# Kernel tuning notes

Measured on AMD Instinct MI355X. Metric: run time of the kernel, lower is better.

Reference implementation:

```python
import jax, jax.numpy as jnp
import numpy as np

NUM_HEADS = 12
EPSILON = 1e-6
SCORE_SCALE = 1.0


def setup_inputs() -> dict:
    key = jax.random.key(0)
    ks = jax.random.split(key, 5)
    B, L, E = 2, 2048, 768
    x = jax.random.normal(ks[0], (B, L, E), dtype=jnp.float32)
    attention_mask = jnp.ones((B, L), dtype=jnp.int32)
    # linear params (lecun-ish scale)
    Wqkv = jax.random.normal(ks[1], (E, 3 * E), dtype=jnp.float32) / np.sqrt(E)
    bqkv = jnp.zeros((3 * E,), dtype=jnp.float32)
    Wout = jax.random.normal(ks[2], (E, E), dtype=jnp.float32) / np.sqrt(E)
    bout = jnp.zeros((E,), dtype=jnp.float32)
    return {"x": x, "attention_mask": attention_mask, "Wqkv": Wqkv,
            "bqkv": bqkv, "Wout": Wout, "bout": bout}


def reference(x, attention_mask, Wqkv, bqkv, Wout, bout):
    B, L, E = x.shape
    H = NUM_HEADS
    D = E // H
    qkv = x @ Wqkv + bqkv                      # [B,L,3E]
    q, k, v = jnp.split(qkv, 3, axis=-1)
    q = q.reshape(B, L, H, D).transpose(0, 2, 1, 3)  # [B,H,L,D]
    k = k.reshape(B, L, H, D).transpose(0, 2, 1, 3)
    v = v.reshape(B, L, H, D).transpose(0, 2, 1, 3)

    dot = jnp.einsum('bhid,bhjd->bhij', q, k)        # [B,H,L,L]
    q_sq = jnp.sum(q * q, axis=-1)[..., :, None]     # [B,H,L,1]
    k_sq = jnp.sum(k * k, axis=-1)[..., None, :]     # [B,H,1,L]
    scores = (dot * dot) / (q_sq + k_sq - 2.0 * dot + EPSILON)
    scores = scores * SCORE_SCALE

    pad = attention_mask[:, None, None, :]           # [B,1,1,L]
    scores = jnp.where(pad == 1, scores, jnp.finfo(scores.dtype).min)

    attn = jax.nn.softmax(scores, axis=-1)
    out = jnp.einsum('bhij,bhjd->bhid', attn, v)     # [B,H,L,D]
    out = out.transpose(0, 2, 1, 3).reshape(B, L, E)
    return out @ Wout + bout
```

## Files before the change

### kernel.cpp

```cpp
#include <hip/hip_runtime.h>
#include <hip/hip_bf16.h>
#include <cstdint>
#include <cstddef>


typedef __bf16 bf16_t;
typedef __bf16 bf16x8 __attribute__((ext_vector_type(8)));
typedef __bf16 bf16x4 __attribute__((ext_vector_type(4)));
typedef float floatx4 __attribute__((ext_vector_type(4)));

#define DEVI static __device__ __forceinline__

#define Bc 2
#define Lc 2048
#define Ec 768
#define Hc 12
#define Dc 64
#define N3c 2304
#define Mc 4096
#define ROWSc (Bc * Hc * Lc)

DEVI void glds16(const bf16_t* g, bf16_t* l) {
  __builtin_amdgcn_global_load_lds(
      (const __attribute__((address_space(1))) void*)g,
      (__attribute__((address_space(3))) void*)l, 16, 0, 0);
}


__global__ __launch_bounds__(256) void k_cvt(const float* __restrict__ in,
                                             bf16_t* __restrict__ out, int n) {
  int i = (blockIdx.x * 256 + threadIdx.x) * 4;
  if (i >= n) return;
  float4 v = *(const float4*)(in + i);
  bf16x4 o;
  o[0] = (bf16_t)v.x; o[1] = (bf16_t)v.y; o[2] = (bf16_t)v.z; o[3] = (bf16_t)v.w;
  *(bf16x4*)(out + i) = o;
}

__global__ __launch_bounds__(256) void k_tc(const float* __restrict__ in,
                                            bf16_t* __restrict__ out, int R, int C) {
  __shared__ float tile[32][33];
  int c0 = blockIdx.x * 32, r0 = blockIdx.y * 32;
  int tx = threadIdx.x, ty = threadIdx.y;
  #pragma unroll
  for (int i = 0; i < 32; i += 8)
    tile[ty + i][tx] = in[(size_t)(r0 + ty + i) * C + c0 + tx];
  __syncthreads();
  #pragma unroll
  for (int i = 0; i < 32; i += 8)
    out[(size_t)(c0 + ty + i) * R + r0 + tx] = (bf16_t)tile[tx][ty + i];
}


DEVI void gemm_core(const bf16_t* __restrict__ A, const bf16_t* __restrict__ Bt,
                    bf16_t* lA, bf16_t* lB, int m0, int n0, floatx4 (&acc)[4][4]) {
  const int tid = threadIdx.x, wave = tid >> 6, lane = tid & 63;
  const int wm = (wave >> 1) * 64, wn = (wave & 1) * 64;
  const int lrow = lane >> 2, lseg = lane & 3;
  const int quad = lane >> 4, r16 = lane & 15;
  for (int kk = 0; kk < 768; kk += 32) {
    glds16(A  + (size_t)(m0 + wave * 32      + lrow) * 768 + kk + lseg * 8, lA + (wave * 32) * 32);
    glds16(A  + (size_t)(m0 + wave * 32 + 16 + lrow) * 768 + kk + lseg * 8, lA + (wave * 32 + 16) * 32);
    glds16(Bt + (size_t)(n0 + wave * 32      + lrow) * 768 + kk + lseg * 8, lB + (wave * 32) * 32);
    glds16(Bt + (size_t)(n0 + wave * 32 + 16 + lrow) * 768 + kk + lseg * 8, lB + (wave * 32 + 16) * 32);
    __syncthreads();
    bf16x8 af[4], bv[4];
    #pragma unroll
    for (int mi = 0; mi < 4; mi++)
      af[mi] = *(const bf16x8*)(lA + (wm + mi * 16 + r16) * 32 + quad * 8);
    #pragma unroll
    for (int ni = 0; ni < 4; ni++)
      bv[ni] = *(const bf16x8*)(lB + (wn + ni * 16 + r16) * 32 + quad * 8);
    #pragma unroll
    for (int mi = 0; mi < 4; mi++)
      #pragma unroll
      for (int ni = 0; ni < 4; ni++)
        acc[mi][ni] = __builtin_amdgcn_mfma_f32_16x16x32_bf16(af[mi], bv[ni], acc[mi][ni], 0, 0, 0);
    __syncthreads();
  }
}

__global__ __launch_bounds__(256) void k_gemm_qkv(
    const bf16_t* __restrict__ A, const bf16_t* __restrict__ Bt,
    const float* __restrict__ bias,
    bf16_t* __restrict__ Qo, bf16_t* __restrict__ Ko, bf16_t* __restrict__ Vo) {
  __shared__ bf16_t lA[128 * 32];
  __shared__ bf16_t lB[128 * 32];
  const int m0 = blockIdx.y * 128, n0 = blockIdx.x * 128;
  const int tid = threadIdx.x, wave = tid >> 6, lane = tid & 63;
  const int wm = (wave >> 1) * 64, wn = (wave & 1) * 64;
  const int quad = lane >> 4, r16 = lane & 15;
  floatx4 acc[4][4] = {};
  gemm_core(A, Bt, lA, lB, m0, n0, acc);

  const int sec = n0 / 768;
  bf16_t* dst = (sec == 0) ? Qo : ((sec == 1) ? Ko : Vo);
  #pragma unroll
  for (int ni = 0; ni < 4; ni++) {
    const int n = n0 + wn + ni * 16 + r16;
    const int nn = n - sec * 768;
    const int h = nn >> 6, d = nn & 63;
    const float bvs = bias[n];
    #pragma unroll
    for (int mi = 0; mi < 4; mi++) {
      #pragma unroll
      for (int reg = 0; reg < 4; reg++) {
        const int m = m0 + wm + mi * 16 + quad * 4 + reg;
        const int b = m >> 11, l = m & 2047;
        const float v = acc[mi][ni][reg] + bvs;
        dst[(((size_t)(b * Hc + h)) * Lc + l) * Dc + d] = (bf16_t)v;
      }
    }
  }
}

__global__ __launch_bounds__(256) void k_gemm_out(
    const bf16_t* __restrict__ A, const bf16_t* __restrict__ Bt,
    const float* __restrict__ bias, float* __restrict__ out) {
  __shared__ bf16_t lA[128 * 32];
  __shared__ bf16_t lB[128 * 32];
  const int m0 = blockIdx.y * 128, n0 = blockIdx.x * 128;
  const int tid = threadIdx.x, wave = tid >> 6, lane = tid & 63;
  const int wm = (wave >> 1) * 64, wn = (wave & 1) * 64;
  const int quad = lane >> 4, r16 = lane & 15;
  floatx4 acc[4][4] = {};
  gemm_core(A, Bt, lA, lB, m0, n0, acc);
  #pragma unroll
  for (int ni = 0; ni < 4; ni++) {
    const int n = n0 + wn + ni * 16 + r16;
    const float bvs = bias[n];
    #pragma unroll
    for (int mi = 0; mi < 4; mi++) {
      #pragma unroll
      for (int reg = 0; reg < 4; reg++) {
        const int m = m0 + wm + mi * 16 + quad * 4 + reg;
        out[(size_t)m * Ec + n] = acc[mi][ni][reg] + bvs;
      }
    }
  }
}

__global__ __launch_bounds__(256) void k_sq(const bf16_t* __restrict__ Q,
                                            const bf16_t* __restrict__ K,
                                            float* __restrict__ qsq, float* __restrict__ ksq) {
  const int row = blockIdx.x * 256 + threadIdx.x;
  const bf16x8* q = (const bf16x8*)(Q + (size_t)row * 64);
  const bf16x8* k = (const bf16x8*)(K + (size_t)row * 64);
  float sq = 0.f, sk = 0.f;
  #pragma unroll
  for (int c = 0; c < 8; c++) {
    bf16x8 vq = q[c], vk = k[c];
    #pragma unroll
    for (int j = 0; j < 8; j++) {
      float a = (float)vq[j]; sq += a * a;
      float b = (float)vk[j]; sk += b * b;
    }
  }
  qsq[row] = sq;
  ksq[row] = sk + 1e-6f;
}

__global__ __launch_bounds__(256) void k_vt(const bf16_t* __restrict__ V,
                                            bf16_t* __restrict__ VT) {
  __shared__ bf16_t t[64][72];
  const int gid = blockIdx.x;
  const int bh = gid >> 5, j0 = (gid & 31) * 64;
  const int tid = threadIdx.x;
  const bf16_t* Vh = V + ((size_t)bh * Lc) * Dc;
  bf16_t* VTh = VT + ((size_t)bh * Dc) * Lc;
  #pragma unroll
  for (int it = 0; it < 2; ++it) {
    int c = tid + it * 256;
    int j = c >> 3, seg = c & 7;
    *(bf16x8*)&t[j][seg * 8] = *(const bf16x8*)(Vh + (size_t)(j0 + j) * 64 + seg * 8);
  }
  __syncthreads();
  #pragma unroll
  for (int it = 0; it < 2; ++it) {
    int c = tid + it * 256;
    int d = c >> 3, jseg = c & 7;
    bf16x8 o;
    #pragma unroll
    for (int u = 0; u < 8; u++) o[u] = t[jseg * 8 + u][d];
    *(bf16x8*)(VTh + (size_t)d * Lc + j0 + jseg * 8) = o;
  }
}

__global__ __launch_bounds__(256) void k_attn(
    const bf16_t* __restrict__ Q, const bf16_t* __restrict__ K,
    const bf16_t* __restrict__ VT, const float* __restrict__ qsq,
    const float* __restrict__ ksq, const int* __restrict__ mask,
    float* __restrict__ Op, float* __restrict__ Mp, float* __restrict__ Lp,
    int nS) {
  __shared__ bf16_t lK[2][4096];
  __shared__ bf16_t lV[2][4096];
  __shared__ bf16_t lP[4][16 * 72];
  const int gid = blockIdx.x;
  const int s = blockIdx.y;
  const int bh = gid >> 5, qt = gid & 31;
  const int b = bh / Hc;
  const int tid = threadIdx.x, wave = tid >> 6, lane = tid & 63;
  const int quad = lane >> 4, r16 = lane & 15;
  const int q0 = qt * 64 + wave * 16;
  const bf16_t* Qh = Q + ((size_t)bh * Lc) * Dc;
  const bf16_t* Kh = K + ((size_t)bh * Lc) * Dc;
  const bf16_t* VTh = VT + ((size_t)bh * Dc) * Lc;
  const float* qsqh = qsq + bh * Lc;
  const float* ksqh = ksq + bh * Lc;
  const int* maskb = mask + b * Lc;
  bf16_t* myP = &lP[wave][0];

  const int kt_lo = (32 * s) / nS * 64;
  const int kt_hi = (32 * (s + 1)) / nS * 64;
  const int nt = (kt_hi - kt_lo) >> 6;

  const int p0 = wave * 64 + lane;
  const int srow = p0 >> 3;
  const int sj = (p0 & 7) ^ (srow & 7);
  const bf16_t* kg0 = Kh + (size_t)(kt_lo + srow) * 64 + sj * 8;
  const bf16_t* kg1 = kg0 + 32 * 64;
  const bf16_t* vg0 = VTh + (size_t)srow * Lc + kt_lo + sj * 8;
  const bf16_t* vg1 = vg0 + 32 * Lc;
  const int ld0 = wave * 64 * 8, ld1 = (256 + wave * 64) * 8;

  const int sl0 = ((quad ^ (r16 & 7)) * 8);
  const int sl1 = sl0 ^ 32;

  bf16x8 qf0 = *(const bf16x8*)(Qh + (size_t)(q0 + r16) * 64 + quad * 8);
  bf16x8 qf1 = *(const bf16x8*)(Qh + (size_t)(q0 + r16) * 64 + 32 + quad * 8);
  const float qs = qsqh[q0 + r16];
  float mi = -1e30f, li = 0.f;
  floatx4 of[4] = {};

  glds16(kg0, &lK[0][ld0]);
  glds16(kg1, &lK[0][ld1]);
  glds16(vg0, &lV[0][ld0]);
  glds16(vg1, &lV[0][ld1]);
  kg0 += 4096; kg1 += 4096; vg0 += 64; vg1 += 64;
  __syncthreads();

  for (int t = 0; t < nt; t++) {
    const int cur = t & 1;
    if (t + 1 < nt) {
      const int nxt = cur ^ 1;
      glds16(kg0, &lK[nxt][ld0]);
      glds16(kg1, &lK[nxt][ld1]);
      glds16(vg0, &lV[nxt][ld0]);
      glds16(vg1, &lV[nxt][ld1]);
      kg0 += 4096; kg1 += 4096; vg0 += 64; vg1 += 64;
    }
    const int kt = kt_lo + t * 64;
    float4 ks4[4];
    int4 mk4[4];
    #pragma unroll
    for (int c = 0; c < 4; c++) {
      ks4[c] = *(const float4*)(ksqh + kt + c * 16 + quad * 4);
      mk4[c] = *(const int4*)(maskb + kt + c * 16 + quad * 4);
    }
    floatx4 dot[4];
    #pragma unroll
    for (int c = 0; c < 4; c++) {
      const int rbase = (c * 16 + r16) * 64;
      bf16x8 kf0 = *(const bf16x8*)(&lK[cur][rbase + sl0]);
      bf16x8 kf1 = *(const bf16x8*)(&lK[cur][rbase + sl1]);
      floatx4 a = {};
      a = __builtin_amdgcn_mfma_f32_16x16x32_bf16(kf0, qf0, a, 0, 0, 0);
      a = __builtin_amdgcn_mfma_f32_16x16x32_bf16(kf1, qf1, a, 0, 0, 0);
      dot[c] = a;
    }
    float sv[4][4];
    float rmax = -1e30f;
    #pragma unroll
    for (int c = 0; c < 4; c++) {
      #pragma unroll
      for (int reg = 0; reg < 4; reg++) {
        const float dd = dot[c][reg];
        const float kss = ((const float*)&ks4[c])[reg];
        const int mk = ((const int*)&mk4[c])[reg];
        const float den = qs + kss - 2.f * dd;
        float sc = dd * dd * __builtin_amdgcn_rcpf(den);
        sc = (mk == 1) ? sc : -1e30f;
        sv[c][reg] = sc;
        rmax = fmaxf(rmax, sc);
      }
    }
    rmax = fmaxf(rmax, __shfl_xor(rmax, 16));
    rmax = fmaxf(rmax, __shfl_xor(rmax, 32));
    const float mnew = fmaxf(mi, rmax);
    const float alpha = __expf(mi - mnew);
    float psum = 0.f;
    #pragma unroll
    for (int c = 0; c < 4; c++) {
      bf16x4 pk;
      #pragma unroll
      for (int reg = 0; reg < 4; reg++) {
        const float p = __expf(sv[c][reg] - mnew);
        psum += p;
        pk[reg] = (bf16_t)p;
      }
      *(bf16x4*)(myP + r16 * 72 + c * 16 + quad * 4) = pk;
    }
    psum += __shfl_xor(psum, 16);
    psum += __shfl_xor(psum, 32);
    li = li * alpha + psum;
    mi = mnew;
    #pragma unroll
    for (int t4 = 0; t4 < 4; t4++) {
      #pragma unroll
      for (int reg = 0; reg < 4; reg++) of[t4][reg] *= alpha;
    }
    bf16x8 pf0 = *(const bf16x8*)(myP + r16 * 72 + quad * 8);
    bf16x8 pf1 = *(const bf16x8*)(myP + r16 * 72 + 32 + quad * 8);
    #pragma unroll
    for (int t4 = 0; t4 < 4; t4++) {
      const int rbase = (t4 * 16 + r16) * 64;
      bf16x8 vf0 = *(const bf16x8*)(&lV[cur][rbase + sl0]);
      bf16x8 vf1 = *(const bf16x8*)(&lV[cur][rbase + sl1]);
      of[t4] = __builtin_amdgcn_mfma_f32_16x16x32_bf16(vf0, pf0, of[t4], 0, 0, 0);
      of[t4] = __builtin_amdgcn_mfma_f32_16x16x32_bf16(vf1, pf1, of[t4], 0, 0, 0);
    }
    __syncthreads();
  }
  const size_t idx = (size_t)s * ROWSc + (size_t)bh * Lc + q0 + r16;
  #pragma unroll
  for (int t4 = 0; t4 < 4; t4++)
    *(float4*)(Op + idx * 64 + t4 * 16 + quad * 4) =
        make_float4(of[t4][0], of[t4][1], of[t4][2], of[t4][3]);
  if (lane < 16) { Mp[idx] = mi; Lp[idx] = li; }
}

__global__ __launch_bounds__(256) void k_merge(
    const float* __restrict__ Op, const float* __restrict__ Mp,
    const float* __restrict__ Lp, bf16_t* __restrict__ AO, int nS) {
  const int t = blockIdx.x * 256 + threadIdx.x;
  const int row = t >> 4, dc = (t & 15) * 4;
  float mmax = -1e30f;
  for (int s = 0; s < nS; s++) mmax = fmaxf(mmax, Mp[(size_t)s * ROWSc + row]);
  float L = 0.f;
  float o0 = 0.f, o1 = 0.f, o2 = 0.f, o3 = 0.f;
  for (int s = 0; s < nS; s++) {
    const size_t idx = (size_t)s * ROWSc + row;
    const float w = __expf(Mp[idx] - mmax);
    L += w * Lp[idx];
    const float4 v = *(const float4*)(Op + idx * 64 + dc);
    o0 += w * v.x; o1 += w * v.y; o2 += w * v.z; o3 += w * v.w;
  }
  const float inv = (L > 0.f) ? __builtin_amdgcn_rcpf(L) : 0.f;
  const int bh = row >> 11, l = row & 2047;
  const int b = bh / Hc, h = bh - b * Hc;
  bf16x4 o;
  o[0] = (bf16_t)(o0 * inv); o[1] = (bf16_t)(o1 * inv);
  o[2] = (bf16_t)(o2 * inv); o[3] = (bf16_t)(o3 * inv);
  *(bf16x4*)(AO + ((size_t)(b * Lc + l)) * Ec + h * 64 + dc) = o;
}


extern "C" void kernel_launch(void* const* d_in, const int* in_sizes, int n_in,
                              void* d_out, int out_size, void* d_ws, size_t ws_size,
                              hipStream_t stream) {
  const float* x    = (const float*)d_in[0];
  const int*   mask = (const int*)d_in[1];
  const float* Wqkv = (const float*)d_in[2];
  const float* bqkv = (const float*)d_in[3];
  const float* Wout = (const float*)d_in[4];
  const float* bout = (const float*)d_in[5];
  float* out = (float*)d_out;

  auto al = [](size_t x) { return (x + 255) & ~(size_t)255; };
  char* ws = (char*)d_ws;
  size_t off = 0;
  auto carve = [&](size_t bytes) -> char* {
    char* p = ws + off;
    off += al(bytes);
    return p;
  };
  bf16_t* WoT = (bf16_t*)carve((size_t)Ec * Ec * 2);
  bf16_t* Qb  = (bf16_t*)carve((size_t)ROWSc * Dc * 2);
  bf16_t* Kb  = (bf16_t*)carve((size_t)ROWSc * Dc * 2);
  bf16_t* VTb = (bf16_t*)carve((size_t)ROWSc * Dc * 2);
  bf16_t* AOb = (bf16_t*)carve((size_t)Mc * Ec * 2);
  float*  qsq = (float*)carve((size_t)ROWSc * 4);
  float*  ksq = (float*)carve((size_t)ROWSc * 4);
  const size_t uni = off;
  bf16_t* xb  = (bf16_t*)(ws + uni);
  bf16_t* WqT = (bf16_t*)(ws + uni + al((size_t)Mc * Ec * 2));
  bf16_t* Vb  = (bf16_t*)(ws + uni + al((size_t)Mc * Ec * 2) + al((size_t)N3c * Ec * 2));
  const size_t ph1 = al((size_t)Mc * Ec * 2) + al((size_t)N3c * Ec * 2) + al((size_t)ROWSc * Dc * 2);
  auto ph2 = [&](int S) {
    return al((size_t)S * ROWSc * Dc * 4) + 2 * al((size_t)S * ROWSc * 4);
  };
  int S = 1;
  {
    size_t need = uni + (ph1 > ph2(2) ? ph1 : ph2(2));
    if (need <= ws_size) S = 2;
  }
  float* Op = (float*)(ws + uni);
  float* Mp = (float*)(ws + uni + al((size_t)S * ROWSc * Dc * 4));
  float* Lp = (float*)(ws + uni + al((size_t)S * ROWSc * Dc * 4) + al((size_t)S * ROWSc * 4));
  (void)in_sizes; (void)n_in; (void)out_size;

  k_cvt<<<(Mc * Ec / 4 + 255) / 256, 256, 0, stream>>>(x, xb, Mc * Ec);
  k_tc<<<dim3(N3c / 32, Ec / 32), dim3(32, 8), 0, stream>>>(Wqkv, WqT, Ec, N3c);
  k_tc<<<dim3(Ec / 32, Ec / 32), dim3(32, 8), 0, stream>>>(Wout, WoT, Ec, Ec);
  k_gemm_qkv<<<dim3(N3c / 128, Mc / 128), 256, 0, stream>>>(xb, WqT, bqkv, Qb, Kb, Vb);
  k_sq<<<ROWSc / 256, 256, 0, stream>>>(Qb, Kb, qsq, ksq);
  k_vt<<<ROWSc / 64, 256, 0, stream>>>(Vb, VTb);
  k_attn<<<dim3(ROWSc / 64, S), 256, 0, stream>>>(Qb, Kb, VTb, qsq, ksq, mask, Op, Mp, Lp, S);
  k_merge<<<ROWSc * 16 / 256, 256, 0, stream>>>(Op, Mp, Lp, AOb, S);
  k_gemm_out<<<dim3(Ec / 128, Mc / 128), 256, 0, stream>>>(AOb, WoT, bout, out);
}
```

Before: 219.3 us.

## Fuse V transpose, mask, and split-K merge into neighbouring kernels

The QKV GEMM epilogue now writes V directly in transposed layout with 4-wide stores, removing the separate transpose kernel. The padding mask is folded into the k-squared array as a negative sentinel, so the attention kernel no longer loads the mask per tile. Attention drops the two-way key split and the merge kernel, normalising and writing bf16 output directly. This removes the partial-output round trip and two launches, but halves the grid of the attention kernel, which can cost occupancy and load balance.

```diff
diff --git a/kernel.cpp b/kernel.cpp
--- a/kernel.cpp
+++ b/kernel.cpp
@@ -83,7 +83,7 @@
 __global__ __launch_bounds__(256) void k_gemm_qkv(
     const bf16_t* __restrict__ A, const bf16_t* __restrict__ Bt,
     const float* __restrict__ bias,
-    bf16_t* __restrict__ Qo, bf16_t* __restrict__ Ko, bf16_t* __restrict__ Vo) {
+    bf16_t* __restrict__ Qo, bf16_t* __restrict__ Ko, bf16_t* __restrict__ VTo) {
   __shared__ bf16_t lA[128 * 32];
   __shared__ bf16_t lB[128 * 32];
   const int m0 = blockIdx.y * 128, n0 = blockIdx.x * 128;
@@ -94,21 +94,40 @@
   gemm_core(A, Bt, lA, lB, m0, n0, acc);
 
   const int sec = n0 / 768;
-  bf16_t* dst = (sec == 0) ? Qo : ((sec == 1) ? Ko : Vo);
-  #pragma unroll
-  for (int ni = 0; ni < 4; ni++) {
-    const int n = n0 + wn + ni * 16 + r16;
-    const int nn = n - sec * 768;
-    const int h = nn >> 6, d = nn & 63;
-    const float bvs = bias[n];
-    #pragma unroll
-    for (int mi = 0; mi < 4; mi++) {
-      #pragma unroll
-      for (int reg = 0; reg < 4; reg++) {
-        const int m = m0 + wm + mi * 16 + quad * 4 + reg;
+  if (sec == 2) {
+    #pragma unroll
+    for (int ni = 0; ni < 4; ni++) {
+      const int n = n0 + wn + ni * 16 + r16;
+      const int nn = n - 1536;
+      const int h = nn >> 6, d = nn & 63;
+      const float bvs = bias[n];
+      #pragma unroll
+      for (int mi = 0; mi < 4; mi++) {
+        const int m = m0 + wm + mi * 16 + quad * 4;
         const int b = m >> 11, l = m & 2047;
-        const float v = acc[mi][ni][reg] + bvs;
-        dst[(((size_t)(b * Hc + h)) * Lc + l) * Dc + d] = (bf16_t)v;
+        bf16x4 o;
+        #pragma unroll
+        for (int reg = 0; reg < 4; reg++) o[reg] = (bf16_t)(acc[mi][ni][reg] + bvs);
+        *(bf16x4*)(VTo + ((size_t)(b * Hc + h) * Dc + d) * Lc + l) = o;
+      }
+    }
+  } else {
+    bf16_t* dst = (sec == 0) ? Qo : Ko;
+    #pragma unroll
+    for (int ni = 0; ni < 4; ni++) {
+      const int n = n0 + wn + ni * 16 + r16;
+      const int nn = n - sec * 768;
+      const int h = nn >> 6, d = nn & 63;
+      const float bvs = bias[n];
+      #pragma unroll
+      for (int mi = 0; mi < 4; mi++) {
+        #pragma unroll
+        for (int reg = 0; reg < 4; reg++) {
+          const int m = m0 + wm + mi * 16 + quad * 4 + reg;
+          const int b = m >> 11, l = m & 2047;
+          const float v = acc[mi][ni][reg] + bvs;
+          dst[(((size_t)(b * Hc + h)) * Lc + l) * Dc + d] = (bf16_t)v;
+        }
       }
     }
   }
@@ -142,6 +161,7 @@
 
 __global__ __launch_bounds__(256) void k_sq(const bf16_t* __restrict__ Q,
                                             const bf16_t* __restrict__ K,
+                                            const int* __restrict__ mask,
                                             float* __restrict__ qsq, float* __restrict__ ksq) {
   const int row = blockIdx.x * 256 + threadIdx.x;
   const bf16x8* q = (const bf16x8*)(Q + (size_t)row * 64);
@@ -156,49 +176,23 @@
       float b = (float)vk[j]; sk += b * b;
     }
   }
+  const int bh = row >> 11, l = row & 2047;
+  const int b = bh / Hc;
+  const int mk = mask[b * Lc + l];
   qsq[row] = sq;
-  ksq[row] = sk + 1e-6f;
-}
-
-__global__ __launch_bounds__(256) void k_vt(const bf16_t* __restrict__ V,
-                                            bf16_t* __restrict__ VT) {
-  __shared__ bf16_t t[64][72];
-  const int gid = blockIdx.x;
-  const int bh = gid >> 5, j0 = (gid & 31) * 64;
-  const int tid = threadIdx.x;
-  const bf16_t* Vh = V + ((size_t)bh * Lc) * Dc;
-  bf16_t* VTh = VT + ((size_t)bh * Dc) * Lc;
-  #pragma unroll
-  for (int it = 0; it < 2; ++it) {
-    int c = tid + it * 256;
-    int j = c >> 3, seg = c & 7;
-    *(bf16x8*)&t[j][seg * 8] = *(const bf16x8*)(Vh + (size_t)(j0 + j) * 64 + seg * 8);
-  }
-  __syncthreads();
-  #pragma unroll
-  for (int it = 0; it < 2; ++it) {
-    int c = tid + it * 256;
-    int d = c >> 3, jseg = c & 7;
-    bf16x8 o;
-    #pragma unroll
-    for (int u = 0; u < 8; u++) o[u] = t[jseg * 8 + u][d];
-    *(bf16x8*)(VTh + (size_t)d * Lc + j0 + jseg * 8) = o;
-  }
+  ksq[row] = (mk == 1) ? (sk + 1e-6f) : -1e30f;
 }
 
 __global__ __launch_bounds__(256) void k_attn(
     const bf16_t* __restrict__ Q, const bf16_t* __restrict__ K,
     const bf16_t* __restrict__ VT, const float* __restrict__ qsq,
-    const float* __restrict__ ksq, const int* __restrict__ mask,
-    float* __restrict__ Op, float* __restrict__ Mp, float* __restrict__ Lp,
-    int nS) {
+    const float* __restrict__ ksq, bf16_t* __restrict__ AO) {
   __shared__ bf16_t lK[2][4096];
   __shared__ bf16_t lV[2][4096];
   __shared__ bf16_t lP[4][16 * 72];
   const int gid = blockIdx.x;
-  const int s = blockIdx.y;
   const int bh = gid >> 5, qt = gid & 31;
-  const int b = bh / Hc;
+  const int b = bh / Hc, h = bh - b * Hc;
   const int tid = threadIdx.x, wave = tid >> 6, lane = tid & 63;
   const int quad = lane >> 4, r16 = lane & 15;
   const int q0 = qt * 64 + wave * 16;
@@ -207,19 +201,14 @@
   const bf16_t* VTh = VT + ((size_t)bh * Dc) * Lc;
   const float* qsqh = qsq + bh * Lc;
   const float* ksqh = ksq + bh * Lc;
-  const int* maskb = mask + b * Lc;
   bf16_t* myP = &lP[wave][0];
-
-  const int kt_lo = (32 * s) / nS * 64;
-  const int kt_hi = (32 * (s + 1)) / nS * 64;
-  const int nt = (kt_hi - kt_lo) >> 6;
 
   const int p0 = wave * 64 + lane;
   const int srow = p0 >> 3;
   const int sj = (p0 & 7) ^ (srow & 7);
-  const bf16_t* kg0 = Kh + (size_t)(kt_lo + srow) * 64 + sj * 8;
+  const bf16_t* kg0 = Kh + (size_t)srow * 64 + sj * 8;
   const bf16_t* kg1 = kg0 + 32 * 64;
-  const bf16_t* vg0 = VTh + (size_t)srow * Lc + kt_lo + sj * 8;
+  const bf16_t* vg0 = VTh + (size_t)srow * Lc + sj * 8;
   const bf16_t* vg1 = vg0 + 32 * Lc;
   const int ld0 = wave * 64 * 8, ld1 = (256 + wave * 64) * 8;
 
@@ -239,6 +228,7 @@
   kg0 += 4096; kg1 += 4096; vg0 += 64; vg1 += 64;
   __syncthreads();
 
+  const int nt = Lc / 64;
   for (int t = 0; t < nt; t++) {
     const int cur = t & 1;
     if (t + 1 < nt) {
@@ -249,14 +239,11 @@
       glds16(vg1, &lV[nxt][ld1]);
       kg0 += 4096; kg1 += 4096; vg0 += 64; vg1 += 64;
     }
-    const int kt = kt_lo + t * 64;
+    const int kt = t * 64;
     float4 ks4[4];
-    int4 mk4[4];
-    #pragma unroll
-    for (int c = 0; c < 4; c++) {
+    #pragma unroll
+    for (int c = 0; c < 4; c++)
       ks4[c] = *(const float4*)(ksqh + kt + c * 16 + quad * 4);
-      mk4[c] = *(const int4*)(maskb + kt + c * 16 + quad * 4);
-    }
     floatx4 dot[4];
     #pragma unroll
     for (int c = 0; c < 4; c++) {
@@ -276,10 +263,9 @@
       for (int reg = 0; reg < 4; reg++) {
         const float dd = dot[c][reg];
         const float kss = ((const float*)&ks4[c])[reg];
-        const int mk = ((const int*)&mk4[c])[reg];
         const float den = qs + kss - 2.f * dd;
         float sc = dd * dd * __builtin_amdgcn_rcpf(den);
-        sc = (mk == 1) ? sc : -1e30f;
+        sc = (kss < 0.f) ? -1e30f : sc;
         sv[c][reg] = sc;
         rmax = fmaxf(rmax, sc);
       }
@@ -321,37 +307,16 @@
     }
     __syncthreads();
   }
-  const size_t idx = (size_t)s * ROWSc + (size_t)bh * Lc + q0 + r16;
-  #pragma unroll
-  for (int t4 = 0; t4 < 4; t4++)
-    *(float4*)(Op + idx * 64 + t4 * 16 + quad * 4) =
-        make_float4(of[t4][0], of[t4][1], of[t4][2], of[t4][3]);
-  if (lane < 16) { Mp[idx] = mi; Lp[idx] = li; }
-}
-
-__global__ __launch_bounds__(256) void k_merge(
-    const float* __restrict__ Op, const float* __restrict__ Mp,
-    const float* __restrict__ Lp, bf16_t* __restrict__ AO, int nS) {
-  const int t = blockIdx.x * 256 + threadIdx.x;
-  const int row = t >> 4, dc = (t & 15) * 4;
-  float mmax = -1e30f;
-  for (int s = 0; s < nS; s++) mmax = fmaxf(mmax, Mp[(size_t)s * ROWSc + row]);
-  float L = 0.f;
-  float o0 = 0.f, o1 = 0.f, o2 = 0.f, o3 = 0.f;
-  for (int s = 0; s < nS; s++) {
-    const size_t idx = (size_t)s * ROWSc + row;
-    const float w = __expf(Mp[idx] - mmax);
-    L += w * Lp[idx];
-    const float4 v = *(const float4*)(Op + idx * 64 + dc);
-    o0 += w * v.x; o1 += w * v.y; o2 += w * v.z; o3 += w * v.w;
-  }
-  const float inv = (L > 0.f) ? __builtin_amdgcn_rcpf(L) : 0.f;
-  const int bh = row >> 11, l = row & 2047;
-  const int b = bh / Hc, h = bh - b * Hc;
-  bf16x4 o;
-  o[0] = (bf16_t)(o0 * inv); o[1] = (bf16_t)(o1 * inv);
-  o[2] = (bf16_t)(o2 * inv); o[3] = (bf16_t)(o3 * inv);
-  *(bf16x4*)(AO + ((size_t)(b * Lc + l)) * Ec + h * 64 + dc) = o;
+  const float inv = (li > 0.f) ? __builtin_amdgcn_rcpf(li) : 0.f;
+  const int l = q0 + r16;
+  bf16_t* aor = AO + ((size_t)(b * Lc + l)) * Ec + h * 64;
+  #pragma unroll
+  for (int t4 = 0; t4 < 4; t4++) {
+    bf16x4 o;
+    #pragma unroll
+    for (int reg = 0; reg < 4; reg++) o[reg] = (bf16_t)(of[t4][reg] * inv);
+    *(bf16x4*)(aor + t4 * 16 + quad * 4) = o;
+  }
 }
 
 
@@ -366,7 +331,7 @@
   const float* bout = (const float*)d_in[5];
   float* out = (float*)d_out;
 
-  auto al = [](size_t x) { return (x + 255) & ~(size_t)255; };
+  auto al = [](size_t v) { return (v + 255) & ~(size_t)255; };
   char* ws = (char*)d_ws;
   size_t off = 0;
   auto carve = [&](size_t bytes) -> char* {
@@ -381,31 +346,15 @@
   bf16_t* AOb = (bf16_t*)carve((size_t)Mc * Ec * 2);
   float*  qsq = (float*)carve((size_t)ROWSc * 4);
   float*  ksq = (float*)carve((size_t)ROWSc * 4);
-  const size_t uni = off;
-  bf16_t* xb  = (bf16_t*)(ws + uni);
-  bf16_t* WqT = (bf16_t*)(ws + uni + al((size_t)Mc * Ec * 2));
-  bf16_t* Vb  = (bf16_t*)(ws + uni + al((size_t)Mc * Ec * 2) + al((size_t)N3c * Ec * 2));
-  const size_t ph1 = al((size_t)Mc * Ec * 2) + al((size_t)N3c * Ec * 2) + al((size_t)ROWSc * Dc * 2);
-  auto ph2 = [&](int S) {
-    return al((size_t)S * ROWSc * Dc * 4) + 2 * al((size_t)S * ROWSc * 4);
-  };
-  int S = 1;
-  {
-    size_t need = uni + (ph1 > ph2(2) ? ph1 : ph2(2));
-    if (need <= ws_size) S = 2;
-  }
-  float* Op = (float*)(ws + uni);
-  float* Mp = (float*)(ws + uni + al((size_t)S * ROWSc * Dc * 4));
-  float* Lp = (float*)(ws + uni + al((size_t)S * ROWSc * Dc * 4) + al((size_t)S * ROWSc * 4));
-  (void)in_sizes; (void)n_in; (void)out_size;
+  bf16_t* xb  = (bf16_t*)carve((size_t)Mc * Ec * 2);
+  bf16_t* WqT = (bf16_t*)carve((size_t)N3c * Ec * 2);
+  (void)in_sizes; (void)n_in; (void)out_size; (void)ws_size;
 
   k_cvt<<<(Mc * Ec / 4 + 255) / 256, 256, 0, stream>>>(x, xb, Mc * Ec);
   k_tc<<<dim3(N3c / 32, Ec / 32), dim3(32, 8), 0, stream>>>(Wqkv, WqT, Ec, N3c);
   k_tc<<<dim3(Ec / 32, Ec / 32), dim3(32, 8), 0, stream>>>(Wout, WoT, Ec, Ec);
-  k_gemm_qkv<<<dim3(N3c / 128, Mc / 128), 256, 0, stream>>>(xb, WqT, bqkv, Qb, Kb, Vb);
-  k_sq<<<ROWSc / 256, 256, 0, stream>>>(Qb, Kb, qsq, ksq);
-  k_vt<<<ROWSc / 64, 256, 0, stream>>>(Vb, VTb);
-  k_attn<<<dim3(ROWSc / 64, S), 256, 0, stream>>>(Qb, Kb, VTb, qsq, ksq, mask, Op, Mp, Lp, S);
-  k_merge<<<ROWSc * 16 / 256, 256, 0, stream>>>(Op, Mp, Lp, AOb, S);
+  k_gemm_qkv<<<dim3(N3c / 128, Mc / 128), 256, 0, stream>>>(xb, WqT, bqkv, Qb, Kb, VTb);
+  k_sq<<<ROWSc / 256, 256, 0, stream>>>(Qb, Kb, mask, qsq, ksq);
+  k_attn<<<ROWSc / 64, 256, 0, stream>>>(Qb, Kb, VTb, qsq, ksq, AOb);
   k_gemm_out<<<dim3(Ec / 128, Mc / 128), 256, 0, stream>>>(AOb, WoT, bout, out);
 }
```

Result: slower. 253.4 us (+15.5%).

## Write V transposed from QKV GEMM epilogue and fold mask into ksq

Applied to the files above, without the earlier changes.

The QKV GEMM epilogue now writes the V section directly in transposed [B,H,D,L] layout with 4-wide bf16 stores, which removes the separate k_vt transpose kernel and its V round-trip through memory. The padding mask is folded into the ksq buffer as a negative sentinel in k_sq, so the attention kernel no longer loads the mask per key tile. The cost is that the Q/K epilogue keeps its scattered scalar stores, and the sentinel check assumes ksq is never otherwise negative.

```diff
diff --git a/kernel.cpp b/kernel.cpp
--- a/kernel.cpp
+++ b/kernel.cpp
@@ -83,7 +83,7 @@
 __global__ __launch_bounds__(256) void k_gemm_qkv(
     const bf16_t* __restrict__ A, const bf16_t* __restrict__ Bt,
     const float* __restrict__ bias,
-    bf16_t* __restrict__ Qo, bf16_t* __restrict__ Ko, bf16_t* __restrict__ Vo) {
+    bf16_t* __restrict__ Qo, bf16_t* __restrict__ Ko, bf16_t* __restrict__ VTo) {
   __shared__ bf16_t lA[128 * 32];
   __shared__ bf16_t lB[128 * 32];
   const int m0 = blockIdx.y * 128, n0 = blockIdx.x * 128;
@@ -94,21 +94,40 @@
   gemm_core(A, Bt, lA, lB, m0, n0, acc);
 
   const int sec = n0 / 768;
-  bf16_t* dst = (sec == 0) ? Qo : ((sec == 1) ? Ko : Vo);
-  #pragma unroll
-  for (int ni = 0; ni < 4; ni++) {
-    const int n = n0 + wn + ni * 16 + r16;
-    const int nn = n - sec * 768;
-    const int h = nn >> 6, d = nn & 63;
-    const float bvs = bias[n];
-    #pragma unroll
-    for (int mi = 0; mi < 4; mi++) {
-      #pragma unroll
-      for (int reg = 0; reg < 4; reg++) {
-        const int m = m0 + wm + mi * 16 + quad * 4 + reg;
+  if (sec == 2) {
+    #pragma unroll
+    for (int ni = 0; ni < 4; ni++) {
+      const int n = n0 + wn + ni * 16 + r16;
+      const int nn = n - 1536;
+      const int h = nn >> 6, d = nn & 63;
+      const float bvs = bias[n];
+      #pragma unroll
+      for (int mi = 0; mi < 4; mi++) {
+        const int m = m0 + wm + mi * 16 + quad * 4;
         const int b = m >> 11, l = m & 2047;
-        const float v = acc[mi][ni][reg] + bvs;
-        dst[(((size_t)(b * Hc + h)) * Lc + l) * Dc + d] = (bf16_t)v;
+        bf16x4 o;
+        #pragma unroll
+        for (int reg = 0; reg < 4; reg++) o[reg] = (bf16_t)(acc[mi][ni][reg] + bvs);
+        *(bf16x4*)(VTo + ((size_t)(b * Hc + h) * Dc + d) * Lc + l) = o;
+      }
+    }
+  } else {
+    bf16_t* dst = (sec == 0) ? Qo : Ko;
+    #pragma unroll
+    for (int ni = 0; ni < 4; ni++) {
+      const int n = n0 + wn + ni * 16 + r16;
+      const int nn = n - sec * 768;
+      const int h = nn >> 6, d = nn & 63;
+      const float bvs = bias[n];
+      #pragma unroll
+      for (int mi = 0; mi < 4; mi++) {
+        #pragma unroll
+        for (int reg = 0; reg < 4; reg++) {
+          const int m = m0 + wm + mi * 16 + quad * 4 + reg;
+          const int b = m >> 11, l = m & 2047;
+          const float v = acc[mi][ni][reg] + bvs;
+          dst[(((size_t)(b * Hc + h)) * Lc + l) * Dc + d] = (bf16_t)v;
+        }
       }
     }
   }
@@ -142,6 +161,7 @@
 
 __global__ __launch_bounds__(256) void k_sq(const bf16_t* __restrict__ Q,
                                             const bf16_t* __restrict__ K,
+                                            const int* __restrict__ mask,
                                             float* __restrict__ qsq, float* __restrict__ ksq) {
   const int row = blockIdx.x * 256 + threadIdx.x;
   const bf16x8* q = (const bf16x8*)(Q + (size_t)row * 64);
@@ -156,40 +176,17 @@
       float b = (float)vk[j]; sk += b * b;
     }
   }
+  const int bh = row >> 11, l = row & 2047;
+  const int b = bh / Hc;
+  const int mk = mask[b * Lc + l];
   qsq[row] = sq;
-  ksq[row] = sk + 1e-6f;
-}
-
-__global__ __launch_bounds__(256) void k_vt(const bf16_t* __restrict__ V,
-                                            bf16_t* __restrict__ VT) {
-  __shared__ bf16_t t[64][72];
-  const int gid = blockIdx.x;
-  const int bh = gid >> 5, j0 = (gid & 31) * 64;
-  const int tid = threadIdx.x;
-  const bf16_t* Vh = V + ((size_t)bh * Lc) * Dc;
-  bf16_t* VTh = VT + ((size_t)bh * Dc) * Lc;
-  #pragma unroll
-  for (int it = 0; it < 2; ++it) {
-    int c = tid + it * 256;
-    int j = c >> 3, seg = c & 7;
-    *(bf16x8*)&t[j][seg * 8] = *(const bf16x8*)(Vh + (size_t)(j0 + j) * 64 + seg * 8);
-  }
-  __syncthreads();
-  #pragma unroll
-  for (int it = 0; it < 2; ++it) {
-    int c = tid + it * 256;
-    int d = c >> 3, jseg = c & 7;
-    bf16x8 o;
-    #pragma unroll
-    for (int u = 0; u < 8; u++) o[u] = t[jseg * 8 + u][d];
-    *(bf16x8*)(VTh + (size_t)d * Lc + j0 + jseg * 8) = o;
-  }
+  ksq[row] = (mk == 1) ? (sk + 1e-6f) : -1e30f;
 }
 
 __global__ __launch_bounds__(256) void k_attn(
     const bf16_t* __restrict__ Q, const bf16_t* __restrict__ K,
     const bf16_t* __restrict__ VT, const float* __restrict__ qsq,
-    const float* __restrict__ ksq, const int* __restrict__ mask,
+    const float* __restrict__ ksq,
     float* __restrict__ Op, float* __restrict__ Mp, float* __restrict__ Lp,
     int nS) {
   __shared__ bf16_t lK[2][4096];
@@ -198,7 +195,6 @@
   const int gid = blockIdx.x;
   const int s = blockIdx.y;
   const int bh = gid >> 5, qt = gid & 31;
-  const int b = bh / Hc;
   const int tid = threadIdx.x, wave = tid >> 6, lane = tid & 63;
   const int quad = lane >> 4, r16 = lane & 15;
   const int q0 = qt * 64 + wave * 16;
@@ -207,7 +203,6 @@
   const bf16_t* VTh = VT + ((size_t)bh * Dc) * Lc;
   const float* qsqh = qsq + bh * Lc;
   const float* ksqh = ksq + bh * Lc;
-  const int* maskb = mask + b * Lc;
   bf16_t* myP = &lP[wave][0];
 
   const int kt_lo = (32 * s) / nS * 64;
@@ -251,12 +246,9 @@
     }
     const int kt = kt_lo + t * 64;
     float4 ks4[4];
-    int4 mk4[4];
-    #pragma unroll
-    for (int c = 0; c < 4; c++) {
+    #pragma unroll
+    for (int c = 0; c < 4; c++)
       ks4[c] = *(const float4*)(ksqh + kt + c * 16 + quad * 4);
-      mk4[c] = *(const int4*)(maskb + kt + c * 16 + quad * 4);
-    }
     floatx4 dot[4];
     #pragma unroll
     for (int c = 0; c < 4; c++) {
@@ -276,10 +268,9 @@
       for (int reg = 0; reg < 4; reg++) {
         const float dd = dot[c][reg];
         const float kss = ((const float*)&ks4[c])[reg];
-        const int mk = ((const int*)&mk4[c])[reg];
         const float den = qs + kss - 2.f * dd;
         float sc = dd * dd * __builtin_amdgcn_rcpf(den);
-        sc = (mk == 1) ? sc : -1e30f;
+        sc = (kss < 0.f) ? -1e30f : sc;
         sv[c][reg] = sc;
         rmax = fmaxf(rmax, sc);
       }
@@ -366,7 +357,7 @@
   const float* bout = (const float*)d_in[5];
   float* out = (float*)d_out;
 
-  auto al = [](size_t x) { return (x + 255) & ~(size_t)255; };
+  auto al = [](size_t v) { return (v + 255) & ~(size_t)255; };
   char* ws = (char*)d_ws;
   size_t off = 0;
   auto carve = [&](size_t bytes) -> char* {
@@ -384,8 +375,7 @@
   const size_t uni = off;
   bf16_t* xb  = (bf16_t*)(ws + uni);
   bf16_t* WqT = (bf16_t*)(ws + uni + al((size_t)Mc * Ec * 2));
-  bf16_t* Vb  = (bf16_t*)(ws + uni + al((size_t)Mc * Ec * 2) + al((size_t)N3c * Ec * 2));
-  const size_t ph1 = al((size_t)Mc * Ec * 2) + al((size_t)N3c * Ec * 2) + al((size_t)ROWSc * Dc * 2);
+  const size_t ph1 = al((size_t)Mc * Ec * 2) + al((size_t)N3c * Ec * 2);
   auto ph2 = [&](int S) {
     return al((size_t)S * ROWSc * Dc * 4) + 2 * al((size_t)S * ROWSc * 4);
   };
@@ -402,10 +392,9 @@
   k_cvt<<<(Mc * Ec / 4 + 255) / 256, 256, 0, stream>>>(x, xb, Mc * Ec);
   k_tc<<<dim3(N3c / 32, Ec / 32), dim3(32, 8), 0, stream>>>(Wqkv, WqT, Ec, N3c);
   k_tc<<<dim3(Ec / 32, Ec / 32), dim3(32, 8), 0, stream>>>(Wout, WoT, Ec, Ec);
-  k_gemm_qkv<<<dim3(N3c / 128, Mc / 128), 256, 0, stream>>>(xb, WqT, bqkv, Qb, Kb, Vb);
-  k_sq<<<ROWSc / 256, 256, 0, stream>>>(Qb, Kb, qsq, ksq);
-  k_vt<<<ROWSc / 64, 256, 0, stream>>>(Vb, VTb);
-  k_attn<<<dim3(ROWSc / 64, S), 256, 0, stream>>>(Qb, Kb, VTb, qsq, ksq, mask, Op, Mp, Lp, S);
+  k_gemm_qkv<<<dim3(N3c / 128, Mc / 128), 256, 0, stream>>>(xb, WqT, bqkv, Qb, Kb, VTb);
+  k_sq<<<ROWSc / 256, 256, 0, stream>>>(Qb, Kb, mask, qsq, ksq);
+  k_attn<<<dim3(ROWSc / 64, S), 256, 0, stream>>>(Qb, Kb, VTb, qsq, ksq, Op, Mp, Lp, S);
   k_merge<<<ROWSc * 16 / 256, 256, 0, stream>>>(Op, Mp, Lp, AOb, S);
   k_gemm_out<<<dim3(Ec / 128, Mc / 128), 256, 0, stream>>>(AOb, WoT, bout, out);
 }
```

Result: slower. 228.4 us (+4.1%).
